# Optimization experiments

Measured on AMD Instinct MI355X. Metric: run time of the kernel, lower is better.

The kernel has to match this reference:

```python
import jax, jax.numpy as jnp
import numpy as np

N = 50000      # nodes
E = 800000     # edges
D = 128        # in_dim == out_dim
H = 8          # heads
DH = D // H    # head dim = 16
BN_EPS = 1e-5


def batch_norm(x, gamma, beta):
    # BatchNorm1d in training mode: biased variance over the node/batch axis.
    mu = jnp.mean(x, axis=0)
    var = jnp.mean((x - mu) ** 2, axis=0)
    return (x - mu) * jax.lax.rsqrt(var + BN_EPS) * gamma + beta


def setup_inputs() -> dict:
    key = jax.random.key(0)
    ks = jax.random.split(key, 16)
    inp = {
        'src': jax.random.randint(ks[0], (E,), 0, N),
        'dst': jax.random.randint(ks[1], (E,), 0, N),
        'h': jax.random.normal(ks[2], (N, D), jnp.float32),
        'e': jax.random.normal(ks[3], (E, D), jnp.float32),
        'h_in': jax.random.normal(ks[4], (N, D), jnp.float32),  # unused: overwritten by h in forward
        # attention projections (bias=False)
        'Wq': jax.random.normal(ks[5], (D, D), jnp.float32) / np.sqrt(D),
        'Wk': jax.random.normal(ks[6], (D, D), jnp.float32) / np.sqrt(D),
        'Wv': jax.random.normal(ks[7], (D, D), jnp.float32) / np.sqrt(D),
        'We': jax.random.normal(ks[8], (D, D), jnp.float32) / np.sqrt(D),
        # sdp_layer (bias=True)
        'W_sdp': jax.random.normal(ks[9], (D, D), jnp.float32) / np.sqrt(D),
        'b_sdp': jnp.zeros((D,), jnp.float32),
        # FFN out_h / out_h_2
        'W_h1': jax.random.normal(ks[10], (D, 2 * D), jnp.float32) / np.sqrt(D),
        'b_h1': jnp.zeros((2 * D,), jnp.float32),
        'W_h2': jax.random.normal(ks[11], (2 * D, D), jnp.float32) / np.sqrt(2 * D),
        'b_h2': jnp.zeros((D,), jnp.float32),
        # batch_norm_1 (shared across both BN applications)
        'bn_gamma': jnp.ones((D,), jnp.float32),
        'bn_beta': jnp.zeros((D,), jnp.float32),
    }
    return inp


def reference(src, dst, h, e, h_in, Wq, Wk, Wv, We, W_sdp, b_sdp,
              W_h1, b_h1, W_h2, b_h2, bn_gamma, bn_beta):
    h_res = h  # h_in = h inside forward

    # --- MultiHeadAttention (default path: all edges real, sum aggregation) ---
    q = (h @ Wq).reshape(N, H, DH)
    k = (h @ Wk).reshape(N, H, DH)
    v = (h @ Wv).reshape(N, H, DH)   # v = v_linear(h_in) with h_in == h
    ef = (e @ We).reshape(E, H, DH)

    # src_dot_dst -> scaling -> imp_exp_attn: elementwise K_src*Q_dst / sqrt(dh) * E
    score = (k[src] * q[dst]) / np.sqrt(DH) * ef          # [E, H, DH]
    # exp('score'): exp(clamp(sum_d score, -5, 5)), keepdim
    score_soft = jnp.exp(jnp.clip(score.sum(-1), -5.0, 5.0))[..., None]  # [E, H, 1]

    aV = jax.ops.segment_sum(v[src] * score_soft, dst, num_segments=N)   # [N, H, DH]
    z = jax.ops.segment_sum(score_soft, dst, num_segments=N)             # [N, H, 1]
    h_attn = (aV / (z + 1e-6)).reshape(N, D)

    # --- EncoderLayer post-attention (dropout=0 -> identity) ---
    hx = h_attn @ W_sdp + b_sdp
    hx = h_res + hx
    hx = batch_norm(hx, bn_gamma, bn_beta)

    h_in2 = hx
    ff = jax.nn.relu(hx @ W_h1 + b_h1) @ W_h2 + b_h2
    hx = h_in2 + ff
    hx = batch_norm(hx, bn_gamma, bn_beta)

    # edge_learning=False: e returned unchanged
    return hx, e
```

## Files before the change

### kernel.cpp

```cpp
#include <hip/hip_runtime.h>
#include <hip/hip_bf16.h>
#include <math.h>

#define N_NODES 50000
#define E_EDGES 800000
#define D_DIM   128
#define H_HEADS 8

typedef __attribute__((ext_vector_type(8))) short short8;
typedef __attribute__((ext_vector_type(4))) float f32x4;
typedef unsigned int   uint_t;
typedef unsigned short ushort_t;

static __device__ __forceinline__ float4 ldg4(const float* p) {
    return *reinterpret_cast<const float4*>(p);
}
static __device__ __forceinline__ ushort_t f2bf(float x) {
    union { float f; uint_t u; } v; v.f = x;
    uint_t r = v.u + 0x7fffu + ((v.u >> 16) & 1u);
    return (ushort_t)(r >> 16);
}
static __device__ __forceinline__ uint_t pk(float lo, float hi) {
    return (uint_t)f2bf(lo) | ((uint_t)f2bf(hi) << 16);
}

__global__ void hist_kernel(const int* __restrict__ dst, int* __restrict__ hist) {
    int i = blockIdx.x * blockDim.x + threadIdx.x;
    if (i < E_EDGES) atomicAdd(&hist[dst[i]], 1);
}

__global__ __launch_bounds__(1024) void scan_kernel(const int* __restrict__ cnt,
                                                    int* __restrict__ start,
                                                    int* __restrict__ cursor) {
    __shared__ int sh[1024];
    const int t = threadIdx.x;
    const int CPT = (N_NODES + 1023) / 1024;
    int lo = t * CPT;
    int hi = lo + CPT; if (hi > N_NODES) hi = N_NODES; if (lo > N_NODES) lo = N_NODES;
    int s = 0;
    for (int i = lo; i < hi; i++) s += cnt[i];
    sh[t] = s;
    __syncthreads();
    for (int off = 1; off < 1024; off <<= 1) {
        int v = (t >= off) ? sh[t - off] : 0;
        __syncthreads();
        sh[t] += v;
        __syncthreads();
    }
    int run = sh[t] - s;
    for (int i = lo; i < hi; i++) {
        start[i]  = run;
        cursor[i] = run;
        run += cnt[i];
    }
    if (t == 1023) start[N_NODES] = sh[1023];
}

__global__ void scatter_kernel(const int* __restrict__ src, const int* __restrict__ dst,
                               int* __restrict__ cursor,
                               int* __restrict__ rank, int* __restrict__ srcs) {
    int i = blockIdx.x * blockDim.x + threadIdx.x;
    if (i < E_EDGES) {
        int p = atomicAdd(&cursor[dst[i]], 1);
        rank[i] = p;
        srcs[p] = src[i];
    }
}

__global__ __launch_bounds__(256) void prep_weights(const float* __restrict__ Wq,
                                                    const float* __restrict__ Wk,
                                                    const float* __restrict__ Wv,
                                                    const float* __restrict__ We,
                                                    const float* __restrict__ Wsdp,
                                                    const float* __restrict__ Wh1,
                                                    const float* __restrict__ Wh2,
                                                    ushort_t* __restrict__ prep) {
    const int b = blockIdx.x;
    const float* W; int ld, cb, kc;
    if (b < 6)       { W = (b < 2 ? Wq : (b < 4 ? Wk : Wv)); ld = 128; cb = 0; kc = b & 1; }
    else if (b < 8)  { W = We;   ld = 128; cb = 0;            kc = b - 6; }
    else if (b < 10) { W = Wsdp; ld = 128; cb = 0;            kc = b - 8; }
    else if (b < 14) { W = Wh1;  ld = 256; cb = (b - 10) >> 1; kc = (b - 10) & 1; }
    else             { W = Wh2;  ld = 128; cb = 0;            kc = b - 14; }
    char* tile = (char*)(prep + (size_t)b * 8192);
    for (int i = threadIdx.x; i < 8192; i += 256) {
        int col = i >> 6, kl = i & 63;
        int k = kc * 64 + kl;
        float v = W[(size_t)k * ld + cb * 128 + col];
        int byte = (col * 128 + kl * 2) ^ ((col & 7) << 4);
        *(ushort_t*)(tile + byte) = f2bf(v);
    }
}

__global__ __launch_bounds__(256) void prep_we_frag(const float* __restrict__ We,
                                                    ushort_t* __restrict__ WeF) {
    int slot = blockIdx.x * 256 + threadIdx.x;
    if (slot < 2048) {
        int lane = slot & 63;
        int kc   = (slot >> 6) & 3;
        int cg   = slot >> 8;
        int col  = cg * 16 + (lane & 15);
        int kb   = kc * 32 + ((lane >> 4) << 3);
#pragma unroll
        for (int j = 0; j < 8; j++)
            WeF[slot * 8 + j] = f2bf(We[(size_t)(kb + j) * 128 + col]);
    }
}

__global__ __launch_bounds__(256) void gemm_bf16(const float* __restrict__ A,
                                                 int M, int K,
                                                 const ushort_t* __restrict__ Bt, int nkc,
                                                 const float* __restrict__ bias,
                                                 const float* __restrict__ resid,
                                                 float* __restrict__ C, int ldc,
                                                 size_t cbStride, int doRelu) {
    __shared__ __align__(16) unsigned char As[16384];
    __shared__ __align__(16) unsigned char Bs[16384];
    const int tid  = threadIdx.x;
    const int lane = tid & 63;
    const int wid  = tid >> 6;
    const int wr   = wid >> 1;
    const int wc   = wid & 1;
    const int cb   = blockIdx.y;
    const int row0 = blockIdx.x * 128;

    f32x4 acc[4][4];
#pragma unroll
    for (int i = 0; i < 4; i++)
#pragma unroll
        for (int j = 0; j < 4; j++) acc[i][j] = (f32x4){0.f, 0.f, 0.f, 0.f};

    for (int kc = 0; kc < nkc; kc++) {
        __syncthreads();
        {
            int row = tid >> 1;
            int kl0 = (tid & 1) * 32;
            int gr  = row0 + row;
            float4 v4[8];
            if (gr < M) {
                const float* ap = &A[(size_t)gr * K + kc * 64 + kl0];
#pragma unroll
                for (int j = 0; j < 8; j++) v4[j] = ldg4(ap + 4 * j);
            } else {
#pragma unroll
                for (int j = 0; j < 8; j++) v4[j] = make_float4(0.f, 0.f, 0.f, 0.f);
            }
            int s = (row & 7) << 4;
#pragma unroll
            for (int j = 0; j < 4; j++) {
                uint4 w;
                w.x = pk(v4[2 * j].x, v4[2 * j].y);
                w.y = pk(v4[2 * j].z, v4[2 * j].w);
                w.z = pk(v4[2 * j + 1].x, v4[2 * j + 1].y);
                w.w = pk(v4[2 * j + 1].z, v4[2 * j + 1].w);
                int byte = (row * 128 + (kl0 + 8 * j) * 2) ^ s;
                *(uint4*)(As + byte) = w;
            }
        }
        {
            const uint4* gB = (const uint4*)(Bt + (size_t)(cb * nkc + kc) * 8192);
#pragma unroll
            for (int j = 0; j < 4; j++) {
                int idx = j * 256 + tid;
                ((uint4*)Bs)[idx] = gB[idx];
            }
        }
        __syncthreads();
#pragma unroll
        for (int k0 = 0; k0 < 64; k0 += 32) {
            short8 a[4], b[4];
#pragma unroll
            for (int mi = 0; mi < 4; mi++) {
                int row = wr * 64 + mi * 16 + (lane & 15);
                int byte = (row * 128 + k0 * 2 + (lane >> 4) * 16) ^ ((row & 7) << 4);
                a[mi] = *(const short8*)(As + byte);
            }
#pragma unroll
            for (int ni = 0; ni < 4; ni++) {
                int col = wc * 64 + ni * 16 + (lane & 15);
                int byte = (col * 128 + k0 * 2 + (lane >> 4) * 16) ^ ((col & 7) << 4);
                b[ni] = *(const short8*)(Bs + byte);
            }
#pragma unroll
            for (int mi = 0; mi < 4; mi++)
#pragma unroll
                for (int ni = 0; ni < 4; ni++)
                    acc[mi][ni] = __builtin_amdgcn_mfma_f32_16x16x32_bf16(a[mi], b[ni], acc[mi][ni], 0, 0, 0);
        }
    }
#pragma unroll
    for (int mi = 0; mi < 4; mi++) {
#pragma unroll
        for (int r = 0; r < 4; r++) {
            int row = row0 + wr * 64 + mi * 16 + ((lane >> 4) << 2) + r;
            if (row < M) {
#pragma unroll
                for (int ni = 0; ni < 4; ni++) {
                    int col = wc * 64 + ni * 16 + (lane & 15);
                    float v = acc[mi][ni][r];
                    if (bias) v += bias[cb * 128 + col];
                    if (doRelu) v = fmaxf(v, 0.f);
                    if (resid) v += resid[(size_t)row * ldc + col];
                    C[cb * cbStride + (size_t)row * ldc + col] = v;
                }
            }
        }
    }
}

__global__ __launch_bounds__(512, 8) void edge_mfma(const float* __restrict__ e,
                                                    const int* __restrict__ src,
                                                    const int* __restrict__ dst,
                                                    const float* __restrict__ Qm,
                                                    const float* __restrict__ Km,
                                                    const ushort_t* __restrict__ WeF,
                                                    const int* __restrict__ rank,
                                                    float* __restrict__ S,
                                                    float* __restrict__ out_e) {
    __shared__ __align__(16) unsigned char Asm[16384];
    __shared__ float sm[64][8];
    const int tid  = threadIdx.x;
    const int lane = tid & 63;
    const int wid  = tid >> 6;
    const int wr   = wid >> 2;
    const int wc   = wid & 3;
    const int e0   = blockIdx.x * 64;

    {
        int row = tid >> 3;
        int c0  = (tid & 7) * 16;
        const float* ep = &e[(size_t)(e0 + row) * 128 + c0];
        float*       op = &out_e[(size_t)(e0 + row) * 128 + c0];
        float4 v4[4];
#pragma unroll
        for (int j = 0; j < 4; j++) v4[j] = ldg4(ep + 4 * j);
#pragma unroll
        for (int j = 0; j < 4; j++) *(float4*)(op + 4 * j) = v4[j];
        int chunk = c0 >> 6;
        int klb   = (c0 & 63) * 2;
        int s     = (row & 7) << 4;
        uint4 w0, w1;
        w0.x = pk(v4[0].x, v4[0].y); w0.y = pk(v4[0].z, v4[0].w);
        w0.z = pk(v4[1].x, v4[1].y); w0.w = pk(v4[1].z, v4[1].w);
        w1.x = pk(v4[2].x, v4[2].y); w1.y = pk(v4[2].z, v4[2].w);
        w1.z = pk(v4[3].x, v4[3].y); w1.w = pk(v4[3].z, v4[3].w);
        *(uint4*)(Asm + chunk * 8192 + ((row * 128 + klb) ^ s))      = w0;
        *(uint4*)(Asm + chunk * 8192 + ((row * 128 + klb + 16) ^ s)) = w1;
    }
    __syncthreads();

    f32x4 acc[2][2];
#pragma unroll
    for (int i = 0; i < 2; i++)
#pragma unroll
        for (int j = 0; j < 2; j++) acc[i][j] = (f32x4){0.f, 0.f, 0.f, 0.f};

#pragma unroll
    for (int k0 = 0; k0 < 128; k0 += 32) {
        int chunk = k0 >> 6;
        int klb   = (k0 & 63) * 2;
        int kc    = k0 >> 5;
        short8 a[2];
#pragma unroll
        for (int mi = 0; mi < 2; mi++) {
            int arow = wr * 32 + mi * 16 + (lane & 15);
            int byte = chunk * 8192 + ((arow * 128 + klb + (lane >> 4) * 16) ^ ((arow & 7) << 4));
            a[mi] = *(const short8*)(Asm + byte);
        }
#pragma unroll
        for (int ni = 0; ni < 2; ni++) {
            int cg = wc * 2 + ni;
            short8 b = *(const short8*)(WeF + ((size_t)((cg * 4 + kc) * 64 + lane)) * 8);
#pragma unroll
            for (int mi = 0; mi < 2; mi++)
                acc[mi][ni] = __builtin_amdgcn_mfma_f32_16x16x32_bf16(a[mi], b, acc[mi][ni], 0, 0, 0);
        }
    }

#pragma unroll
    for (int mi = 0; mi < 2; mi++) {
        int rows[4], sidx[4], didx[4];
#pragma unroll
        for (int r = 0; r < 4; r++) {
            rows[r] = e0 + wr * 32 + mi * 16 + ((lane >> 4) << 2) + r;
            sidx[r] = src[rows[r]];
            didx[r] = dst[rows[r]];
        }
#pragma unroll
        for (int ni = 0; ni < 2; ni++) {
            int head = wc * 2 + ni;
            int col  = head * 16 + (lane & 15);
            float pv[4];
#pragma unroll
            for (int r = 0; r < 4; r++) {
                float kv = Km[(size_t)sidx[r] * 128 + col];
                float qv = Qm[(size_t)didx[r] * 128 + col];
                pv[r] = acc[mi][ni][r] * kv * qv;
            }
#pragma unroll
            for (int off = 1; off < 16; off <<= 1)
#pragma unroll
                for (int r = 0; r < 4; r++) pv[r] += __shfl_xor(pv[r], off, 64);
            if ((lane & 15) == 0) {
#pragma unroll
                for (int r = 0; r < 4; r++) {
                    float v = fminf(fmaxf(0.25f * pv[r], -5.f), 5.f);
                    sm[rows[r] - e0][head] = __expf(v);
                }
            }
        }
    }
    __syncthreads();
    if (tid < 64) {
        int rk = rank[e0 + tid];
        float4 a0 = *(const float4*)&sm[tid][0];
        float4 a1 = *(const float4*)&sm[tid][4];
        *(float4*)&S[(size_t)rk * 8]     = a0;
        *(float4*)&S[(size_t)rk * 8 + 4] = a1;
    }
}

__global__ __launch_bounds__(128) void agg_kernel(const float* __restrict__ V,
                                                  const float* __restrict__ S,
                                                  const int* __restrict__ start,
                                                  const int* __restrict__ srcs,
                                                  float* __restrict__ HA) {
    const int n = blockIdx.x;
    const int t = threadIdx.x;
    const int h = t >> 4;
    const int s0 = start[n];
    const int s1 = start[n + 1];
    float acc = 0.f, z = 0.f;
    int i = s0;
    for (; i + 4 <= s1; i += 4) {
        int  n0 = srcs[i], n1 = srcs[i + 1], n2 = srcs[i + 2], n3 = srcs[i + 3];
        float sv0 = S[(size_t)i * 8 + h];
        float sv1 = S[(size_t)(i + 1) * 8 + h];
        float sv2 = S[(size_t)(i + 2) * 8 + h];
        float sv3 = S[(size_t)(i + 3) * 8 + h];
        float v0 = V[(size_t)n0 * 128 + t];
        float v1 = V[(size_t)n1 * 128 + t];
        float v2 = V[(size_t)n2 * 128 + t];
        float v3 = V[(size_t)n3 * 128 + t];
        acc = fmaf(sv0, v0, acc); acc = fmaf(sv1, v1, acc);
        acc = fmaf(sv2, v2, acc); acc = fmaf(sv3, v3, acc);
        z += sv0 + sv1 + sv2 + sv3;
    }
    for (; i < s1; i++) {
        int ns = srcs[i];
        float sv = S[(size_t)i * 8 + h];
        acc = fmaf(sv, V[(size_t)ns * 128 + t], acc);
        z += sv;
    }
    HA[(size_t)n * 128 + t] = acc / (z + 1e-6f);
}

__global__ __launch_bounds__(256) void bn_stats(const float* __restrict__ X,
                                                float* __restrict__ sums) {
    __shared__ float s1[256], s2[256];
    const int tid = threadIdx.x;
    float a1 = 0.f, a2 = 0.f;
    const size_t total = (size_t)N_NODES * 128;
    for (size_t i = (size_t)blockIdx.x * 256 + tid; i < total; i += (size_t)gridDim.x * 256) {
        float v = X[i];
        a1 += v;
        a2 += v * v;
    }
    s1[tid] = a1; s2[tid] = a2;
    __syncthreads();
    if (tid < 128) {
        a1 = s1[tid] + s1[tid + 128];
        a2 = s2[tid] + s2[tid + 128];
        atomicAdd(&sums[tid], a1);
        atomicAdd(&sums[128 + tid], a2);
    }
}

__global__ void bn_finalize(const float* __restrict__ sums, float* __restrict__ mu_rstd) {
    int c = threadIdx.x;
    float mu  = sums[c] * (1.f / (float)N_NODES);
    float var = sums[128 + c] * (1.f / (float)N_NODES) - mu * mu;
    mu_rstd[c]       = mu;
    mu_rstd[128 + c] = rsqrtf(var + 1e-5f);
}

__global__ __launch_bounds__(256) void bn_apply(const float* __restrict__ X,
                                                const float* __restrict__ mu_rstd,
                                                const float* __restrict__ gamma,
                                                const float* __restrict__ beta,
                                                float* __restrict__ Y) {
    const size_t total = (size_t)N_NODES * 128;
    const size_t step = (size_t)gridDim.x * blockDim.x * 4;
    for (size_t i = ((size_t)blockIdx.x * blockDim.x + threadIdx.x) * 4; i < total; i += step) {
        float4 x = ldg4(&X[i]);
        int c = (int)(i & 127);
        float4 y;
        y.x = (x.x - mu_rstd[c + 0]) * mu_rstd[128 + c + 0] * gamma[c + 0] + beta[c + 0];
        y.y = (x.y - mu_rstd[c + 1]) * mu_rstd[128 + c + 1] * gamma[c + 1] + beta[c + 1];
        y.z = (x.z - mu_rstd[c + 2]) * mu_rstd[128 + c + 2] * gamma[c + 2] + beta[c + 2];
        y.w = (x.w - mu_rstd[c + 3]) * mu_rstd[128 + c + 3] * gamma[c + 3] + beta[c + 3];
        *reinterpret_cast<float4*>(&Y[i]) = y;
    }
}

extern "C" void kernel_launch(void* const* d_in, const int* in_sizes, int n_in,
                              void* d_out, int out_size, void* d_ws, size_t ws_size,
                              hipStream_t stream) {
    (void)in_sizes; (void)n_in; (void)out_size; (void)ws_size;
    const int*   src   = (const int*)d_in[0];
    const int*   dst   = (const int*)d_in[1];
    const float* h     = (const float*)d_in[2];
    const float* e     = (const float*)d_in[3];
    const float* Wq    = (const float*)d_in[5];
    const float* Wk    = (const float*)d_in[6];
    const float* Wv    = (const float*)d_in[7];
    const float* We    = (const float*)d_in[8];
    const float* Wsdp  = (const float*)d_in[9];
    const float* bsdp  = (const float*)d_in[10];
    const float* Wh1   = (const float*)d_in[11];
    const float* bh1   = (const float*)d_in[12];
    const float* Wh2   = (const float*)d_in[13];
    const float* bh2   = (const float*)d_in[14];
    const float* gamma = (const float*)d_in[15];
    const float* beta  = (const float*)d_in[16];
    float* out = (float*)d_out;

    float* ws = (float*)d_ws;
    const size_t NM = (size_t)N_NODES * 128;
    float* Qb    = ws;
    float* Kb    = ws + NM;
    float* Vb    = ws + 2 * NM;
    float* Sb    = ws + 3 * NM;
    float* T1    = ws + 4 * NM;
    float* STATS = ws + 6 * NM;
    int* hist   = (int*)(STATS + 1024);
    int* startp = hist + N_NODES;
    int* cursor = startp + N_NODES + 1;
    ushort_t* prep = (ushort_t*)(((uintptr_t)(cursor + N_NODES) + 255) & ~(uintptr_t)255);
    ushort_t* WeF  = prep + (size_t)18 * 8192;

    int* rank = (int*)T1;
    int* srcs = rank + E_EDGES;

    float* sums1 = STATS;
    float* mr1   = STATS + 256;
    float* sums2 = STATS + 512;
    float* mr2   = STATS + 768;

    prep_weights<<<18, 256, 0, stream>>>(Wq, Wk, Wv, We, Wsdp, Wh1, Wh2, prep);
    prep_we_frag<<<8, 256, 0, stream>>>(We, WeF);

    hipMemsetAsync(STATS, 0, (1024 + N_NODES) * sizeof(float), stream);

    hist_kernel<<<(E_EDGES + 255) / 256, 256, 0, stream>>>(dst, hist);
    scan_kernel<<<1, 1024, 0, stream>>>(hist, startp, cursor);
    scatter_kernel<<<(E_EDGES + 255) / 256, 256, 0, stream>>>(src, dst, cursor, rank, srcs);

    const int rowTiles = (N_NODES + 127) / 128;

    gemm_bf16<<<dim3(rowTiles, 3), 256, 0, stream>>>(h, N_NODES, 128, prep, 2,
                                                     nullptr, nullptr, Qb, 128, NM, 0);

    edge_mfma<<<E_EDGES / 64, 512, 0, stream>>>(e, src, dst, Qb, Kb, WeF,
                                                rank, Sb, out + NM);

    agg_kernel<<<N_NODES, 128, 0, stream>>>(Vb, Sb, startp, srcs, Qb);

    gemm_bf16<<<dim3(rowTiles, 1), 256, 0, stream>>>(Qb, N_NODES, 128, prep + (size_t)8 * 8192, 2,
                                                     bsdp, h, Kb, 128, 0, 0);

    bn_stats<<<512, 256, 0, stream>>>(Kb, sums1);
    bn_finalize<<<1, 128, 0, stream>>>(sums1, mr1);
    bn_apply<<<2048, 256, 0, stream>>>(Kb, mr1, gamma, beta, Vb);

    gemm_bf16<<<dim3(rowTiles, 2), 256, 0, stream>>>(Vb, N_NODES, 128, prep + (size_t)10 * 8192, 2,
                                                     bh1, nullptr, T1, 256, 128, 1);
    gemm_bf16<<<dim3(rowTiles, 1), 256, 0, stream>>>(T1, N_NODES, 256, prep + (size_t)14 * 8192, 4,
                                                     bh2, Vb, Kb, 128, 0, 0);

    bn_stats<<<512, 256, 0, stream>>>(Kb, sums2);
    bn_finalize<<<1, 128, 0, stream>>>(sums2, mr2);
    bn_apply<<<2048, 256, 0, stream>>>(Kb, mr2, gamma, beta, out);
}
```

Measured before the change: 858.5 us.

## Hoist gathers in edge kernel, use nontemporal edge I/O, 64-row GEMM tiles

The edge kernel now loads the src/dst indices, rank and the K·Q gathered products up front, before the MFMA projection, so the gather latency overlaps with the e load and the matrix work. The 0.25 scale is folded into the precomputed product. The e read and the out_e copy use nontemporal loads and stores to reduce cache pollution. Launch bounds are lowered from 8 to 6 waves to make room for the extra registers. The GEMM is templated on row tile size, and the single-column-block GEMMs use 64-row tiles so more blocks fill the GPU, at the cost of less B-tile reuse.

```diff
diff --git a/kernel.cpp b/kernel.cpp
--- a/kernel.cpp
+++ b/kernel.cpp
@@ -14,6 +14,14 @@
 
 static __device__ __forceinline__ float4 ldg4(const float* p) {
     return *reinterpret_cast<const float4*>(p);
+}
+static __device__ __forceinline__ float4 ldg4_nt(const float* p) {
+    f32x4 v = __builtin_nontemporal_load(reinterpret_cast<const f32x4*>(p));
+    return make_float4(v.x, v.y, v.z, v.w);
+}
+static __device__ __forceinline__ void st4_nt(float* p, float4 v) {
+    f32x4 w = (f32x4){v.x, v.y, v.z, v.w};
+    __builtin_nontemporal_store(w, reinterpret_cast<f32x4*>(p));
 }
 static __device__ __forceinline__ ushort_t f2bf(float x) {
     union { float f; uint_t u; } v; v.f = x;
@@ -107,6 +115,7 @@
     }
 }
 
+template<int ROWS>
 __global__ __launch_bounds__(256) void gemm_bf16(const float* __restrict__ A,
                                                  int M, int K,
                                                  const ushort_t* __restrict__ Bt, int nkc,
@@ -114,7 +123,10 @@
                                                  const float* __restrict__ resid,
                                                  float* __restrict__ C, int ldc,
                                                  size_t cbStride, int doRelu) {
-    __shared__ __align__(16) unsigned char As[16384];
+    constexpr int MI  = ROWS / 32;
+    constexpr int TPR = 256 / ROWS;
+    constexpr int KPT = 64 / TPR;
+    __shared__ __align__(16) unsigned char As[ROWS * 128];
     __shared__ __align__(16) unsigned char Bs[16384];
     const int tid  = threadIdx.x;
     const int lane = tid & 63;
@@ -122,32 +134,32 @@
     const int wr   = wid >> 1;
     const int wc   = wid & 1;
     const int cb   = blockIdx.y;
-    const int row0 = blockIdx.x * 128;
-
-    f32x4 acc[4][4];
-#pragma unroll
-    for (int i = 0; i < 4; i++)
+    const int row0 = blockIdx.x * ROWS;
+
+    f32x4 acc[MI][4];
+#pragma unroll
+    for (int i = 0; i < MI; i++)
 #pragma unroll
         for (int j = 0; j < 4; j++) acc[i][j] = (f32x4){0.f, 0.f, 0.f, 0.f};
 
     for (int kc = 0; kc < nkc; kc++) {
         __syncthreads();
         {
-            int row = tid >> 1;
-            int kl0 = (tid & 1) * 32;
+            int row = tid / TPR;
+            int kl0 = (tid % TPR) * KPT;
             int gr  = row0 + row;
-            float4 v4[8];
+            float4 v4[KPT / 4];
             if (gr < M) {
                 const float* ap = &A[(size_t)gr * K + kc * 64 + kl0];
 #pragma unroll
-                for (int j = 0; j < 8; j++) v4[j] = ldg4(ap + 4 * j);
+                for (int j = 0; j < KPT / 4; j++) v4[j] = ldg4(ap + 4 * j);
             } else {
 #pragma unroll
-                for (int j = 0; j < 8; j++) v4[j] = make_float4(0.f, 0.f, 0.f, 0.f);
+                for (int j = 0; j < KPT / 4; j++) v4[j] = make_float4(0.f, 0.f, 0.f, 0.f);
             }
             int s = (row & 7) << 4;
 #pragma unroll
-            for (int j = 0; j < 4; j++) {
+            for (int j = 0; j < KPT / 8; j++) {
                 uint4 w;
                 w.x = pk(v4[2 * j].x, v4[2 * j].y);
                 w.y = pk(v4[2 * j].z, v4[2 * j].w);
@@ -168,10 +180,10 @@
         __syncthreads();
 #pragma unroll
         for (int k0 = 0; k0 < 64; k0 += 32) {
-            short8 a[4], b[4];
-#pragma unroll
-            for (int mi = 0; mi < 4; mi++) {
-                int row = wr * 64 + mi * 16 + (lane & 15);
+            short8 a[MI], b[4];
+#pragma unroll
+            for (int mi = 0; mi < MI; mi++) {
+                int row = wr * (ROWS / 2) + mi * 16 + (lane & 15);
                 int byte = (row * 128 + k0 * 2 + (lane >> 4) * 16) ^ ((row & 7) << 4);
                 a[mi] = *(const short8*)(As + byte);
             }
@@ -182,17 +194,17 @@
                 b[ni] = *(const short8*)(Bs + byte);
             }
 #pragma unroll
-            for (int mi = 0; mi < 4; mi++)
+            for (int mi = 0; mi < MI; mi++)
 #pragma unroll
                 for (int ni = 0; ni < 4; ni++)
                     acc[mi][ni] = __builtin_amdgcn_mfma_f32_16x16x32_bf16(a[mi], b[ni], acc[mi][ni], 0, 0, 0);
         }
     }
 #pragma unroll
-    for (int mi = 0; mi < 4; mi++) {
+    for (int mi = 0; mi < MI; mi++) {
 #pragma unroll
         for (int r = 0; r < 4; r++) {
-            int row = row0 + wr * 64 + mi * 16 + ((lane >> 4) << 2) + r;
+            int row = row0 + wr * (ROWS / 2) + mi * 16 + ((lane >> 4) << 2) + r;
             if (row < M) {
 #pragma unroll
                 for (int ni = 0; ni < 4; ni++) {
@@ -208,7 +220,7 @@
     }
 }
 
-__global__ __launch_bounds__(512, 8) void edge_mfma(const float* __restrict__ e,
+__global__ __launch_bounds__(512, 6) void edge_mfma(const float* __restrict__ e,
                                                     const int* __restrict__ src,
                                                     const int* __restrict__ dst,
                                                     const float* __restrict__ Qm,
@@ -226,16 +238,43 @@
     const int wc   = wid & 3;
     const int e0   = blockIdx.x * 64;
 
+    int sidx[2][4], didx[2][4];
+#pragma unroll
+    for (int mi = 0; mi < 2; mi++) {
+        int rb = e0 + wr * 32 + mi * 16 + ((lane >> 4) << 2);
+#pragma unroll
+        for (int r = 0; r < 4; r++) {
+            sidx[mi][r] = src[rb + r];
+            didx[mi][r] = dst[rb + r];
+        }
+    }
+    int rk = (tid < 64) ? rank[e0 + tid] : 0;
+
+    const int row = tid >> 3;
+    const int c0  = (tid & 7) * 16;
+    const float* ep = &e[(size_t)(e0 + row) * 128 + c0];
+    float4 v4[4];
+#pragma unroll
+    for (int j = 0; j < 4; j++) v4[j] = ldg4_nt(ep + 4 * j);
+
+    float kq[2][2][4];
+#pragma unroll
+    for (int mi = 0; mi < 2; mi++)
+#pragma unroll
+        for (int ni = 0; ni < 2; ni++) {
+            const int col = (wc * 2 + ni) * 16 + (lane & 15);
+#pragma unroll
+            for (int r = 0; r < 4; r++) {
+                float kv = Km[(size_t)sidx[mi][r] * 128 + col];
+                float qv = Qm[(size_t)didx[mi][r] * 128 + col];
+                kq[mi][ni][r] = kv * qv * 0.25f;
+            }
+        }
+
     {
-        int row = tid >> 3;
-        int c0  = (tid & 7) * 16;
-        const float* ep = &e[(size_t)(e0 + row) * 128 + c0];
-        float*       op = &out_e[(size_t)(e0 + row) * 128 + c0];
-        float4 v4[4];
-#pragma unroll
-        for (int j = 0; j < 4; j++) v4[j] = ldg4(ep + 4 * j);
-#pragma unroll
-        for (int j = 0; j < 4; j++) *(float4*)(op + 4 * j) = v4[j];
+        float* op = &out_e[(size_t)(e0 + row) * 128 + c0];
+#pragma unroll
+        for (int j = 0; j < 4; j++) st4_nt(op + 4 * j, v4[j]);
         int chunk = c0 >> 6;
         int klb   = (c0 & 63) * 2;
         int s     = (row & 7) << 4;
@@ -279,40 +318,28 @@
 
 #pragma unroll
     for (int mi = 0; mi < 2; mi++) {
-        int rows[4], sidx[4], didx[4];
-#pragma unroll
-        for (int r = 0; r < 4; r++) {
-            rows[r] = e0 + wr * 32 + mi * 16 + ((lane >> 4) << 2) + r;
-            sidx[r] = src[rows[r]];
-            didx[r] = dst[rows[r]];
-        }
 #pragma unroll
         for (int ni = 0; ni < 2; ni++) {
-            int head = wc * 2 + ni;
-            int col  = head * 16 + (lane & 15);
             float pv[4];
 #pragma unroll
-            for (int r = 0; r < 4; r++) {
-                float kv = Km[(size_t)sidx[r] * 128 + col];
-                float qv = Qm[(size_t)didx[r] * 128 + col];
-                pv[r] = acc[mi][ni][r] * kv * qv;
-            }
+            for (int r = 0; r < 4; r++) pv[r] = acc[mi][ni][r] * kq[mi][ni][r];
 #pragma unroll
             for (int off = 1; off < 16; off <<= 1)
 #pragma unroll
                 for (int r = 0; r < 4; r++) pv[r] += __shfl_xor(pv[r], off, 64);
             if ((lane & 15) == 0) {
+                const int head = wc * 2 + ni;
+                const int er0  = wr * 32 + mi * 16 + ((lane >> 4) << 2);
 #pragma unroll
                 for (int r = 0; r < 4; r++) {
-                    float v = fminf(fmaxf(0.25f * pv[r], -5.f), 5.f);
-                    sm[rows[r] - e0][head] = __expf(v);
+                    float v = fminf(fmaxf(pv[r], -5.f), 5.f);
+                    sm[er0 + r][head] = __expf(v);
                 }
             }
         }
     }
     __syncthreads();
     if (tid < 64) {
-        int rk = rank[e0 + tid];
         float4 a0 = *(const float4*)&sm[tid][0];
         float4 a1 = *(const float4*)&sm[tid][4];
         *(float4*)&S[(size_t)rk * 8]     = a0;
@@ -456,26 +483,27 @@
     scan_kernel<<<1, 1024, 0, stream>>>(hist, startp, cursor);
     scatter_kernel<<<(E_EDGES + 255) / 256, 256, 0, stream>>>(src, dst, cursor, rank, srcs);
 
-    const int rowTiles = (N_NODES + 127) / 128;
-
-    gemm_bf16<<<dim3(rowTiles, 3), 256, 0, stream>>>(h, N_NODES, 128, prep, 2,
-                                                     nullptr, nullptr, Qb, 128, NM, 0);
+    const int rt128 = (N_NODES + 127) / 128;
+    const int rt64  = (N_NODES + 63) / 64;
+
+    gemm_bf16<128><<<dim3(rt128, 3), 256, 0, stream>>>(h, N_NODES, 128, prep, 2,
+                                                       nullptr, nullptr, Qb, 128, NM, 0);
 
     edge_mfma<<<E_EDGES / 64, 512, 0, stream>>>(e, src, dst, Qb, Kb, WeF,
                                                 rank, Sb, out + NM);
 
     agg_kernel<<<N_NODES, 128, 0, stream>>>(Vb, Sb, startp, srcs, Qb);
 
-    gemm_bf16<<<dim3(rowTiles, 1), 256, 0, stream>>>(Qb, N_NODES, 128, prep + (size_t)8 * 8192, 2,
+    gemm_bf16<64><<<dim3(rt64, 1), 256, 0, stream>>>(Qb, N_NODES, 128, prep + (size_t)8 * 8192, 2,
                                                      bsdp, h, Kb, 128, 0, 0);
 
     bn_stats<<<512, 256, 0, stream>>>(Kb, sums1);
     bn_finalize<<<1, 128, 0, stream>>>(sums1, mr1);
     bn_apply<<<2048, 256, 0, stream>>>(Kb, mr1, gamma, beta, Vb);
 
-    gemm_bf16<<<dim3(rowTiles, 2), 256, 0, stream>>>(Vb, N_NODES, 128, prep + (size_t)10 * 8192, 2,
-                                                     bh1, nullptr, T1, 256, 128, 1);
-    gemm_bf16<<<dim3(rowTiles, 1), 256, 0, stream>>>(T1, N_NODES, 256, prep + (size_t)14 * 8192, 4,
+    gemm_bf16<128><<<dim3(rt128, 2), 256, 0, stream>>>(Vb, N_NODES, 128, prep + (size_t)10 * 8192, 2,
+                                                       bh1, nullptr, T1, 256, 128, 1);
+    gemm_bf16<64><<<dim3(rt64, 1), 256, 0, stream>>>(T1, N_NODES, 256, prep + (size_t)14 * 8192, 4,
                                                      bh2, Vb, Kb, 128, 0, 0);
 
     bn_stats<<<512, 256, 0, stream>>>(Kb, sums2);
```

After: 870.6 us. No clear change (+1.4%).
